# Kernel tuning notes

Measured on AMD Instinct MI355X. Metric: run time of the kernel, lower is better.

The kernel has to match this reference:

```python
import jax, jax.numpy as jnp
import numpy as np

N = 4096; B = 32; LATENT = 16; UNITS = 64; NNZ = 65536; K = 2; M = 2 * K + 1

def _spmm(rows, cols, vals, x):
    # sparse [N,N] @ dense [N,FB] via gather + segment_sum
    return jax.ops.segment_sum(vals[:, None] * x[cols], rows, num_segments=N)

def _gconv(y, supports, W, b):
    # y: (B, N*F) -> Chebyshev-style diffusion over each support, then dense projection
    F = y.shape[1] // N
    x0 = y.reshape(B, N, F).transpose(1, 2, 0).reshape(N, F * B)
    xs = [x0]
    for rows, cols, vals in supports:
        x1 = _spmm(rows, cols, vals, x0)
        xs.append(x1)
        xk1, xk2 = x1, x0
        for _ in range(2, K + 1):
            x2 = 2.0 * _spmm(rows, cols, vals, xk1) - xk2
            xs.append(x2)
            xk1, xk2 = x2, xk1
    # [M,N,F,B] -> [B,N,F,M] -> [B*N, F*M], matching torch permute/reshape
    x = jnp.stack(xs).reshape(M, N, F, B).transpose(3, 1, 2, 0).reshape(B * N, F * M)
    return (x @ W + b).reshape(B, N * W.shape[1])

def setup_inputs():
    key = jax.random.key(0)
    ks = jax.random.split(key, 8)
    r = jax.random.randint(ks[0], (NNZ,), 0, N)
    c = jax.random.randint(ks[1], (NNZ,), 0, N)
    v = jax.random.uniform(ks[2], (NNZ,)) + 0.1
    d_row = jax.ops.segment_sum(v, r, num_segments=N)
    d_col = jax.ops.segment_sum(v, c, num_segments=N)
    inv_row = jnp.where(d_row > 0, 1.0 / d_row, 0.0)
    inv_col = jnp.where(d_col > 0, 1.0 / d_col, 0.0)
    # support1 = (D_out^{-1} A)^T ; support2 = (D_in^{-1} A^T)^T  (COO triples)
    s1_rows, s1_cols, s1_vals = c, r, v * inv_row[r]
    s2_rows, s2_cols, s2_vals = r, c, v * inv_col[c]
    def xavier(k, shape):
        scale = np.sqrt(2.0 / (shape[0] + shape[1])).astype(np.float32)
        return jax.random.normal(k, shape, dtype=jnp.float32) * scale
    return {
        "t_local": 0,
        "y": jax.random.normal(ks[3], (B, N * LATENT), dtype=jnp.float32),
        "W_theta": xavier(ks[4], (LATENT * M, LATENT)),
        "b_lat": jnp.ones((LATENT,), jnp.float32),  # bias_start=1.0; shared (LayerParams keys biases by length)
        "W_hid": xavier(ks[5], (LATENT * M, UNITS)),
        "b_hid": jnp.zeros((UNITS,), jnp.float32),
        "W_out": xavier(ks[6], (UNITS * M, LATENT)),
        "s1_rows": s1_rows, "s1_cols": s1_cols, "s1_vals": s1_vals,
        "s2_rows": s2_rows, "s2_cols": s2_cols, "s2_vals": s2_vals,
    }

def reference(t_local, y, W_theta, b_lat, W_hid, b_hid, W_out,
              s1_rows, s1_cols, s1_vals, s2_rows, s2_cols, s2_vals):
    supports = [(s1_rows, s1_cols, s1_vals), (s2_rows, s2_cols, s2_vals)]
    theta = jax.nn.sigmoid(_gconv(y, supports, W_theta, b_lat))
    c = jnp.tanh(_gconv(y, supports, W_hid, b_hid))   # gen_layers = 1
    c = jnp.tanh(_gconv(c, supports, W_out, b_lat))   # shared bias of length latent_dim
    return -theta * c
```

## Files before the change

### kernel.cpp

```cpp
#include <hip/hip_runtime.h>
#include <stdint.h>

#define NN    4096
#define BB    32
#define NNZE  65536
#define WA    512
#define WB    2048
#define WD    512

typedef __attribute__((ext_vector_type(8))) short bf16x8;
typedef __attribute__((ext_vector_type(4))) float f32x4;

__device__ __forceinline__ float bf2f(unsigned int h) {
    union { unsigned int u; float f; } c; c.u = h << 16; return c.f;
}
__device__ __forceinline__ unsigned int f2bf(float f) {
    union { float ff; unsigned int u; } c; c.ff = f;
    return (c.u + 0x7fffu + ((c.u >> 16) & 1u)) >> 16;
}

__global__ void hist2_kernel(const int* __restrict__ r1, const int* __restrict__ r2,
                             int* __restrict__ cnt1, int* __restrict__ cnt2) {
    int e = blockIdx.x * blockDim.x + threadIdx.x;
    if (e < NNZE) atomicAdd(&cnt1[r1[e]], 1);
    else          atomicAdd(&cnt2[r2[e - NNZE]], 1);
}

__global__ void scan2_kernel(int* cur1, int* rp1, int* cur2, int* rp2) {
    int* cur = (blockIdx.x == 0) ? cur1 : cur2;
    int* rp  = (blockIdx.x == 0) ? rp1  : rp2;
    __shared__ int part[256];
    int t = threadIdx.x;
    int base = t * 16;
    int loc[16];
    int s = 0;
#pragma unroll
    for (int i = 0; i < 16; ++i) { loc[i] = s; s += cur[base + i]; }
    part[t] = s;
    __syncthreads();
    for (int off = 1; off < 256; off <<= 1) {
        int v = 0;
        if (t >= off) v = part[t - off];
        __syncthreads();
        part[t] += v;
        __syncthreads();
    }
    int excl = (t == 0) ? 0 : part[t - 1];
#pragma unroll
    for (int i = 0; i < 16; ++i) rp[base + i] = excl + loc[i];
    __syncthreads();
#pragma unroll
    for (int i = 0; i < 16; ++i) cur[base + i] = rp[base + i];
    if (t == 255) rp[4096] = part[255];
}

__global__ void scatter2_kernel(const int* __restrict__ r1, const int* __restrict__ c1, const float* __restrict__ v1,
                                const int* __restrict__ r2, const int* __restrict__ c2, const float* __restrict__ v2,
                                int* __restrict__ cur1, int* __restrict__ cur2,
                                int* __restrict__ ecol1, float* __restrict__ eval1,
                                int* __restrict__ ecol2, float* __restrict__ eval2) {
    int e = blockIdx.x * blockDim.x + threadIdx.x;
    if (e < NNZE) {
        int pos = atomicAdd(&cur1[r1[e]], 1);
        ecol1[pos] = c1[e]; eval1[pos] = v1[e];
    } else {
        int ee = e - NNZE;
        int pos = atomicAdd(&cur2[r2[ee]], 1);
        ecol2[pos] = c2[ee]; eval2[pos] = v2[ee];
    }
}

__global__ void transA_kernel(const float* __restrict__ y, unsigned short* __restrict__ x0h) {
    int t = threadIdx.x, n = blockIdx.x;
    int b = t & 31, q = t >> 5;
    float4 y4 = *(const float4*)(y + (size_t)b * (NN * 16) + n * 16 + 4 * q);
    uint2 o;
    o.x = f2bf(y4.x) | (f2bf(y4.y) << 16);
    o.y = f2bf(y4.z) | (f2bf(y4.w) << 16);
    *(uint2*)(x0h + (size_t)n * WA + b * 16 + 4 * q) = o;
}

struct SpmmDesc {
    const unsigned short* in;
    const unsigned short* prev;
    float* outF;
    unsigned short* outH;
    const int* rp; const int* ecol; const float* eval;
    float alpha, beta;
};

__launch_bounds__(64)
__global__ void spmmD_kernel(SpmmDesc q0, SpmmDesc q1, SpmmDesc q2, SpmmDesc q3, int ninst) {
    __shared__ int scol[64];
    __shared__ float sval[64];
    int blk = blockIdx.x;
    int xcd = blk & 7;
    int idx = blk >> 3;
    int spx = 8 / ninst;
    int inst = xcd / spx;
    int sub  = xcd - inst * spx;
    int row  = sub * (NN / spx) + idx;
    SpmmDesc q = (inst == 0) ? q0 : (inst == 1) ? q1 : (inst == 2) ? q2 : q3;
    int t = threadIdx.x;
    int beg = q.rp[row], end = q.rp[row + 1];
    float acc[8];
#pragma unroll
    for (int k = 0; k < 8; ++k) acc[k] = 0.f;
    for (int i0 = beg; i0 < end; i0 += 64) {
        int nn = end - i0; if (nn > 64) nn = 64;
        __syncthreads();
        if (t < nn) { scol[t] = q.ecol[i0 + t]; sval[t] = q.eval[i0 + t]; }
        __syncthreads();
#pragma unroll 4
        for (int j = 0; j < nn; ++j) {
            uint4 xv = ((const uint4*)(q.in + (size_t)scol[j] * WD))[t];
            float v = sval[j];
            acc[0] += v * bf2f(xv.x & 0xffffu);
            acc[1] += v * bf2f(xv.x >> 16);
            acc[2] += v * bf2f(xv.y & 0xffffu);
            acc[3] += v * bf2f(xv.y >> 16);
            acc[4] += v * bf2f(xv.z & 0xffffu);
            acc[5] += v * bf2f(xv.z >> 16);
            acc[6] += v * bf2f(xv.w & 0xffffu);
            acc[7] += v * bf2f(xv.w >> 16);
        }
    }
    float r[8];
#pragma unroll
    for (int k = 0; k < 8; ++k) r[k] = q.alpha * acc[k];
    if (q.prev) {
        uint4 pv = ((const uint4*)(q.prev + (size_t)row * WD))[t];
        r[0] += q.beta * bf2f(pv.x & 0xffffu);
        r[1] += q.beta * bf2f(pv.x >> 16);
        r[2] += q.beta * bf2f(pv.y & 0xffffu);
        r[3] += q.beta * bf2f(pv.y >> 16);
        r[4] += q.beta * bf2f(pv.z & 0xffffu);
        r[5] += q.beta * bf2f(pv.z >> 16);
        r[6] += q.beta * bf2f(pv.w & 0xffffu);
        r[7] += q.beta * bf2f(pv.w >> 16);
    }
    if (q.outF) {
        float* po = q.outF + (size_t)row * WD + t * 8;
        *(float4*)(po)     = make_float4(r[0], r[1], r[2], r[3]);
        *(float4*)(po + 4) = make_float4(r[4], r[5], r[6], r[7]);
    } else {
        uint4 o;
        o.x = f2bf(r[0]) | (f2bf(r[1]) << 16);
        o.y = f2bf(r[2]) | (f2bf(r[3]) << 16);
        o.z = f2bf(r[4]) | (f2bf(r[5]) << 16);
        o.w = f2bf(r[6]) | (f2bf(r[7]) << 16);
        ((uint4*)(q.outH + (size_t)row * WD))[t] = o;
    }
}

__launch_bounds__(256)
__global__ void projA_mfma(const unsigned short* __restrict__ xh,
                           const float* __restrict__ Wtheta, const float* __restrict__ Whid,
                           const float* __restrict__ b_hid,
                           float* __restrict__ theta,
                           unsigned short* __restrict__ c) {
    __shared__ __align__(16) unsigned short sW[80 * 104];
    int t = threadIdx.x;
    for (int i = t; i < 80 * 96; i += 256) {
        int col = i / 96, k = i - col * 96;
        int m = k >> 4, f = k & 15;
        float v = 0.f;
        if (m < 5) v = (col < 16) ? Wtheta[(f * 5 + m) * 16 + col]
                                  : Whid[(f * 5 + m) * 64 + (col - 16)];
        sW[col * 104 + k] = (unsigned short)f2bf(v);
    }
    __syncthreads();
    int lane = t & 63, w = t >> 6;
    int r = lane & 15, g = lane >> 4;
    bf16x8 wf[5][3];
#pragma unroll
    for (int ct = 0; ct < 5; ++ct)
#pragma unroll
        for (int kt = 0; kt < 3; ++kt)
            wf[ct][kt] = *(const bf16x8*)(sW + (ct * 16 + r) * 104 + kt * 32 + g * 8);
    float bh[4];
#pragma unroll
    for (int ct = 0; ct < 4; ++ct) bh[ct] = b_hid[ct * 16 + r];

    for (int i = 0; i < 2; ++i) {
        int n = blockIdx.x * 8 + w * 2 + i;
        f32x4 acc[2][5];
#pragma unroll
        for (int bt = 0; bt < 2; ++bt)
#pragma unroll
            for (int ct = 0; ct < 5; ++ct)
                acc[bt][ct] = (f32x4){0.f, 0.f, 0.f, 0.f};
#pragma unroll
        for (int kt = 0; kt < 3; ++kt) {
            bf16x8 a[2];
            int m = kt * 2 + (g >> 1);
#pragma unroll
            for (int bt = 0; bt < 2; ++bt) {
                bf16x8 av = {0, 0, 0, 0, 0, 0, 0, 0};
                if (m < 5)
                    av = *(const bf16x8*)(xh + ((size_t)m * NN + n) * WA
                                          + (bt * 16 + r) * 16 + (g & 1) * 8);
                a[bt] = av;
            }
#pragma unroll
            for (int bt = 0; bt < 2; ++bt)
#pragma unroll
                for (int ct = 0; ct < 5; ++ct)
                    acc[bt][ct] = __builtin_amdgcn_mfma_f32_16x16x32_bf16(
                        a[bt], wf[ct][kt], acc[bt][ct], 0, 0, 0);
        }
#pragma unroll
        for (int bt = 0; bt < 2; ++bt) {
#pragma unroll
            for (int reg = 0; reg < 4; ++reg) {
                int b = bt * 16 + g * 4 + reg;
                theta[(size_t)n * 512 + b * 16 + r] = acc[bt][0][reg];
            }
#pragma unroll
            for (int ct = 1; ct < 5; ++ct) {
                int u = (ct - 1) * 16 + r;
#pragma unroll
                for (int reg = 0; reg < 4; ++reg) {
                    int b = bt * 16 + g * 4 + reg;
                    float hv = tanhf(acc[bt][ct][reg] + bh[ct - 1]);
                    c[(size_t)n * WB + b * 64 + u] = (unsigned short)f2bf(hv);
                }
            }
        }
    }
}

__launch_bounds__(256)
__global__ void preproj_mfma(const unsigned short* __restrict__ c,
                             const float* __restrict__ Wout,
                             float* __restrict__ d0,
                             unsigned short* __restrict__ dd1, unsigned short* __restrict__ dd2,
                             unsigned short* __restrict__ dd3, unsigned short* __restrict__ dd4) {
    __shared__ __align__(16) unsigned short sW[80 * 72];
    int t = threadIdx.x;
    for (int i = t; i < 80 * 64; i += 256) {
        int col = i >> 6, k = i & 63;
        int m = col >> 4, up = col & 15;
        sW[col * 72 + k] = (unsigned short)f2bf(Wout[(k * 5 + m) * 16 + up]);
    }
    __syncthreads();
    int lane = t & 63, w = t >> 6;
    int r = lane & 15, g = lane >> 4;
    bf16x8 wf[5][2];
#pragma unroll
    for (int ct = 0; ct < 5; ++ct)
#pragma unroll
        for (int kt = 0; kt < 2; ++kt)
            wf[ct][kt] = *(const bf16x8*)(sW + (ct * 16 + r) * 72 + kt * 32 + g * 8);

    for (int i = 0; i < 2; ++i) {
        int n = blockIdx.x * 8 + w * 2 + i;
        f32x4 acc[2][5];
#pragma unroll
        for (int bt = 0; bt < 2; ++bt)
#pragma unroll
            for (int ct = 0; ct < 5; ++ct)
                acc[bt][ct] = (f32x4){0.f, 0.f, 0.f, 0.f};
#pragma unroll
        for (int kt = 0; kt < 2; ++kt) {
            bf16x8 a[2];
#pragma unroll
            for (int bt = 0; bt < 2; ++bt)
                a[bt] = *(const bf16x8*)(c + (size_t)n * WB + (bt * 16 + r) * 64
                                         + kt * 32 + g * 8);
#pragma unroll
            for (int bt = 0; bt < 2; ++bt)
#pragma unroll
                for (int ct = 0; ct < 5; ++ct)
                    acc[bt][ct] = __builtin_amdgcn_mfma_f32_16x16x32_bf16(
                        a[bt], wf[ct][kt], acc[bt][ct], 0, 0, 0);
        }
#pragma unroll
        for (int bt = 0; bt < 2; ++bt) {
#pragma unroll
            for (int reg = 0; reg < 4; ++reg) {
                int b = bt * 16 + g * 4 + reg;
                d0[(size_t)n * WD + b * 16 + r] = acc[bt][0][reg];
            }
#pragma unroll
            for (int ct = 1; ct < 5; ++ct) {
                unsigned short* dp = (ct == 1) ? dd1 : (ct == 2) ? dd2 : (ct == 3) ? dd3 : dd4;
#pragma unroll
                for (int reg = 0; reg < 4; ++reg) {
                    int b = bt * 16 + g * 4 + reg;
                    dp[(size_t)n * WD + b * 16 + r] = (unsigned short)f2bf(acc[bt][ct][reg]);
                }
            }
        }
    }
}

__global__ void final2_kernel(const float* __restrict__ theta, const float* __restrict__ d0,
                              const float* __restrict__ w1, const float* __restrict__ z2,
                              const float* __restrict__ w3, const float* __restrict__ z4,
                              const float* __restrict__ b_lat, float* __restrict__ out) {
    int i4 = blockIdx.x * blockDim.x + threadIdx.x;
    size_t i = (size_t)i4 * 4;
    int u = (int)(i & 15);
    int b = (int)((i >> 4) & 31);
    int n = (int)(i >> 9);
    float4 tv = *(const float4*)(theta + i);
    float4 a0 = *(const float4*)(d0 + i);
    float4 a1 = *(const float4*)(w1 + i);
    float4 a2 = *(const float4*)(z2 + i);
    float4 a3 = *(const float4*)(w3 + i);
    float4 a4 = *(const float4*)(z4 + i);
    float4 bl = *(const float4*)(b_lat + u);
    float sx = a0.x + a1.x + a2.x + a3.x + a4.x + bl.x;
    float sy = a0.y + a1.y + a2.y + a3.y + a4.y + bl.y;
    float sz = a0.z + a1.z + a2.z + a3.z + a4.z + bl.z;
    float sw = a0.w + a1.w + a2.w + a3.w + a4.w + bl.w;
    float4 res;
    res.x = -(1.f / (1.f + expf(-(tv.x + bl.x)))) * tanhf(sx);
    res.y = -(1.f / (1.f + expf(-(tv.y + bl.y)))) * tanhf(sy);
    res.z = -(1.f / (1.f + expf(-(tv.z + bl.z)))) * tanhf(sz);
    res.w = -(1.f / (1.f + expf(-(tv.w + bl.w)))) * tanhf(sw);
    *(float4*)(out + ((size_t)b * NN + n) * 16 + u) = res;
}

extern "C" void kernel_launch(void* const* d_in, const int* in_sizes, int n_in,
                              void* d_out, int out_size, void* d_ws, size_t ws_size,
                              hipStream_t stream) {
    const float* y      = (const float*)d_in[1];
    const float* Wtheta = (const float*)d_in[2];
    const float* b_lat  = (const float*)d_in[3];
    const float* Whid   = (const float*)d_in[4];
    const float* b_hid  = (const float*)d_in[5];
    const float* Wout   = (const float*)d_in[6];
    const int*   r1     = (const int*)d_in[7];
    const int*   c1     = (const int*)d_in[8];
    const float* v1     = (const float*)d_in[9];
    const int*   r2     = (const int*)d_in[10];
    const int*   c2     = (const int*)d_in[11];
    const float* v2     = (const float*)d_in[12];
    float* out = (float*)d_out;

    char* ws = (char*)d_ws;
    size_t off = 0;
    auto alloc = [&](size_t bytes) -> char* {
        char* p = ws + off;
        off += (bytes + 255) & ~(size_t)255;
        return p;
    };
    int*   rp1   = (int*)alloc(4097 * 4);
    int*   rp2   = (int*)alloc(4097 * 4);
    int*   cur1  = (int*)alloc(4096 * 4);
    int*   cur2  = (int*)alloc(4096 * 4);
    int*   ecol1 = (int*)alloc(NNZE * 4);
    float* eval1 = (float*)alloc(NNZE * 4);
    int*   ecol2 = (int*)alloc(NNZE * 4);
    float* eval2 = (float*)alloc(NNZE * 4);
    unsigned short* xh = (unsigned short*)alloc((size_t)5 * NN * WA * 2);
    float* theta = (float*)alloc((size_t)NN * 512 * 4);
    char*  creg  = alloc((size_t)NN * WB * 2);
    float* d0 = (float*)alloc((size_t)NN * WD * 4);
    unsigned short* w2h = (unsigned short*)alloc((size_t)NN * WD * 2);
    unsigned short* w4h = (unsigned short*)alloc((size_t)NN * WD * 2);
    float* z2 = (float*)alloc((size_t)NN * WD * 4);
    float* z4 = (float*)alloc((size_t)NN * WD * 4);
    if (off > ws_size) return;

    unsigned short* x0h = xh;
    unsigned short* x1h = xh + (size_t)1 * NN * WA;
    unsigned short* x2h = xh + (size_t)2 * NN * WA;
    unsigned short* x3h = xh + (size_t)3 * NN * WA;
    unsigned short* x4h = xh + (size_t)4 * NN * WA;
    unsigned short* cbuf = (unsigned short*)creg;
    unsigned short* dd1 = (unsigned short*)((char*)xh + ((size_t)0  << 20));
    unsigned short* dd2 = (unsigned short*)((char*)xh + ((size_t)4  << 20));
    unsigned short* dd3 = (unsigned short*)((char*)xh + ((size_t)8  << 20));
    unsigned short* dd4 = (unsigned short*)((char*)xh + ((size_t)12 << 20));
    float* w1 = (float*)creg;
    float* w3 = (float*)(creg + ((size_t)8 << 20));

    hipMemsetAsync(cur1, 0, 2 * 4096 * 4, stream);
    hist2_kernel<<<2 * NNZE / 256, 256, 0, stream>>>(r1, r2, cur1, cur2);
    scan2_kernel<<<2, 256, 0, stream>>>(cur1, rp1, cur2, rp2);
    scatter2_kernel<<<2 * NNZE / 256, 256, 0, stream>>>(r1, c1, v1, r2, c2, v2,
                                                        cur1, cur2, ecol1, eval1, ecol2, eval2);

    transA_kernel<<<NN, 128, 0, stream>>>(y, x0h);
    {
        SpmmDesc a0 = { x0h, nullptr, nullptr, x1h, rp1, ecol1, eval1, 1.f, 0.f };
        SpmmDesc a1 = { x0h, nullptr, nullptr, x3h, rp2, ecol2, eval2, 1.f, 0.f };
        spmmD_kernel<<<2 * NN, 64, 0, stream>>>(a0, a1, a0, a1, 2);
    }
    {
        SpmmDesc a0 = { x1h, x0h, nullptr, x2h, rp1, ecol1, eval1, 2.f, -1.f };
        SpmmDesc a1 = { x3h, x0h, nullptr, x4h, rp2, ecol2, eval2, 2.f, -1.f };
        spmmD_kernel<<<2 * NN, 64, 0, stream>>>(a0, a1, a0, a1, 2);
    }
    projA_mfma<<<NN / 8, 256, 0, stream>>>(xh, Wtheta, Whid, b_hid, theta, cbuf);

    preproj_mfma<<<NN / 8, 256, 0, stream>>>(cbuf, Wout, d0, dd1, dd2, dd3, dd4);
    {
        SpmmDesc a0 = { dd1, nullptr, w1, nullptr, rp1, ecol1, eval1, 1.f, 0.f };
        SpmmDesc a1 = { dd2, nullptr, nullptr, w2h, rp1, ecol1, eval1, 1.f, 0.f };
        SpmmDesc a2 = { dd3, nullptr, w3, nullptr, rp2, ecol2, eval2, 1.f, 0.f };
        SpmmDesc a3 = { dd4, nullptr, nullptr, w4h, rp2, ecol2, eval2, 1.f, 0.f };
        spmmD_kernel<<<4 * NN, 64, 0, stream>>>(a0, a1, a2, a3, 4);
    }
    {
        SpmmDesc b0 = { w2h, dd2, z2, nullptr, rp1, ecol1, eval1, 2.f, -1.f };
        SpmmDesc b1 = { w4h, dd4, z4, nullptr, rp2, ecol2, eval2, 2.f, -1.f };
        spmmD_kernel<<<2 * NN, 64, 0, stream>>>(b0, b1, b0, b1, 2);
    }

    final2_kernel<<<(NN * WD) / 4 / 256, 256, 0, stream>>>(theta, d0, w1, z2, w3, z4, b_lat, out);
}
```

Baseline: 219.4 us.

## Refactor final diffusion via Horner-style SpMM chain and fuse into epilogue

Rewrites the last graph-conv's Chebyshev sum so each support needs one SpMM producing g = 2·S·dd2 + dd1 and a second SpMM applied to g, removing one SpMM pass per support plus the fp32 intermediates w1/w3/z2/z4. The second SpMM over both supports is fused with the sigmoid/tanh epilogue, which also removes the separate final elementwise kernel and its six full-size reads. In exchange, the intermediate g is kept in bf16, which can add rounding error. Each row's combined work now runs in one 64-thread block across both supports, giving fewer and longer blocks.

```diff
diff --git a/kernel.cpp b/kernel.cpp
--- a/kernel.cpp
+++ b/kernel.cpp
@@ -295,32 +295,75 @@
     }
 }
 
-__global__ void final2_kernel(const float* __restrict__ theta, const float* __restrict__ d0,
-                              const float* __restrict__ w1, const float* __restrict__ z2,
-                              const float* __restrict__ w3, const float* __restrict__ z4,
-                              const float* __restrict__ b_lat, float* __restrict__ out) {
-    int i4 = blockIdx.x * blockDim.x + threadIdx.x;
-    size_t i = (size_t)i4 * 4;
-    int u = (int)(i & 15);
-    int b = (int)((i >> 4) & 31);
-    int n = (int)(i >> 9);
-    float4 tv = *(const float4*)(theta + i);
-    float4 a0 = *(const float4*)(d0 + i);
-    float4 a1 = *(const float4*)(w1 + i);
-    float4 a2 = *(const float4*)(z2 + i);
-    float4 a3 = *(const float4*)(w3 + i);
-    float4 a4 = *(const float4*)(z4 + i);
-    float4 bl = *(const float4*)(b_lat + u);
-    float sx = a0.x + a1.x + a2.x + a3.x + a4.x + bl.x;
-    float sy = a0.y + a1.y + a2.y + a3.y + a4.y + bl.y;
-    float sz = a0.z + a1.z + a2.z + a3.z + a4.z + bl.z;
-    float sw = a0.w + a1.w + a2.w + a3.w + a4.w + bl.w;
-    float4 res;
-    res.x = -(1.f / (1.f + expf(-(tv.x + bl.x)))) * tanhf(sx);
-    res.y = -(1.f / (1.f + expf(-(tv.y + bl.y)))) * tanhf(sy);
-    res.z = -(1.f / (1.f + expf(-(tv.z + bl.z)))) * tanhf(sz);
-    res.w = -(1.f / (1.f + expf(-(tv.w + bl.w)))) * tanhf(sw);
-    *(float4*)(out + ((size_t)b * NN + n) * 16 + u) = res;
+__launch_bounds__(64)
+__global__ void finalspmm_kernel(const unsigned short* __restrict__ g1, const unsigned short* __restrict__ g3,
+                                 const int* __restrict__ rp1, const int* __restrict__ ecol1, const float* __restrict__ eval1,
+                                 const int* __restrict__ rp2, const int* __restrict__ ecol2, const float* __restrict__ eval2,
+                                 const float* __restrict__ theta, const float* __restrict__ d0,
+                                 const unsigned short* __restrict__ dd2, const unsigned short* __restrict__ dd4,
+                                 const float* __restrict__ b_lat, float* __restrict__ out) {
+    __shared__ int scol[64];
+    __shared__ float sval[64];
+    int blk = blockIdx.x;
+    int row = (blk & 7) * 512 + (blk >> 3);
+    int t = threadIdx.x;
+    float h[8];
+#pragma unroll
+    for (int k = 0; k < 8; ++k) h[k] = 0.f;
+#pragma unroll
+    for (int s = 0; s < 2; ++s) {
+        const int* rp = s ? rp2 : rp1;
+        const int* ecol = s ? ecol2 : ecol1;
+        const float* eval = s ? eval2 : eval1;
+        const unsigned short* gin = s ? g3 : g1;
+        int beg = rp[row], end = rp[row + 1];
+        for (int i0 = beg; i0 < end; i0 += 64) {
+            int nn = end - i0; if (nn > 64) nn = 64;
+            __syncthreads();
+            if (t < nn) { scol[t] = ecol[i0 + t]; sval[t] = eval[i0 + t]; }
+            __syncthreads();
+#pragma unroll 4
+            for (int j = 0; j < nn; ++j) {
+                uint4 xv = ((const uint4*)(gin + (size_t)scol[j] * WD))[t];
+                float v = sval[j];
+                h[0] += v * bf2f(xv.x & 0xffffu);
+                h[1] += v * bf2f(xv.x >> 16);
+                h[2] += v * bf2f(xv.y & 0xffffu);
+                h[3] += v * bf2f(xv.y >> 16);
+                h[4] += v * bf2f(xv.z & 0xffffu);
+                h[5] += v * bf2f(xv.z >> 16);
+                h[6] += v * bf2f(xv.w & 0xffffu);
+                h[7] += v * bf2f(xv.w >> 16);
+            }
+        }
+    }
+    size_t base = (size_t)row * WD + t * 8;
+    float4 dA = *(const float4*)(d0 + base);
+    float4 dB = *(const float4*)(d0 + base + 4);
+    uint4 p2 = *(const uint4*)(dd2 + base);
+    uint4 p4 = *(const uint4*)(dd4 + base);
+    float4 tA = *(const float4*)(theta + base);
+    float4 tB = *(const float4*)(theta + base + 4);
+    float4 blA = *(const float4*)(b_lat + (t & 1) * 8);
+    float4 blB = *(const float4*)(b_lat + (t & 1) * 8 + 4);
+    float tot[8], th[8];
+    tot[0] = dA.x - bf2f(p2.x & 0xffffu) - bf2f(p4.x & 0xffffu) + h[0] + blA.x;
+    tot[1] = dA.y - bf2f(p2.x >> 16)     - bf2f(p4.x >> 16)     + h[1] + blA.y;
+    tot[2] = dA.z - bf2f(p2.y & 0xffffu) - bf2f(p4.y & 0xffffu) + h[2] + blA.z;
+    tot[3] = dA.w - bf2f(p2.y >> 16)     - bf2f(p4.y >> 16)     + h[3] + blA.w;
+    tot[4] = dB.x - bf2f(p2.z & 0xffffu) - bf2f(p4.z & 0xffffu) + h[4] + blB.x;
+    tot[5] = dB.y - bf2f(p2.z >> 16)     - bf2f(p4.z >> 16)     + h[5] + blB.y;
+    tot[6] = dB.z - bf2f(p2.w & 0xffffu) - bf2f(p4.w & 0xffffu) + h[6] + blB.z;
+    tot[7] = dB.w - bf2f(p2.w >> 16)     - bf2f(p4.w >> 16)     + h[7] + blB.w;
+    th[0] = tA.x + blA.x; th[1] = tA.y + blA.y; th[2] = tA.z + blA.z; th[3] = tA.w + blA.w;
+    th[4] = tB.x + blB.x; th[5] = tB.y + blB.y; th[6] = tB.z + blB.z; th[7] = tB.w + blB.w;
+    float res[8];
+#pragma unroll
+    for (int j = 0; j < 8; ++j)
+        res[j] = -(1.f / (1.f + expf(-th[j]))) * tanhf(tot[j]);
+    float* po = out + ((size_t)(t >> 1) * NN + row) * 16 + (t & 1) * 8;
+    *(float4*)(po)     = make_float4(res[0], res[1], res[2], res[3]);
+    *(float4*)(po + 4) = make_float4(res[4], res[5], res[6], res[7]);
 }
 
 extern "C" void kernel_launch(void* const* d_in, const int* in_sizes, int n_in,
@@ -359,10 +402,8 @@
     float* theta = (float*)alloc((size_t)NN * 512 * 4);
     char*  creg  = alloc((size_t)NN * WB * 2);
     float* d0 = (float*)alloc((size_t)NN * WD * 4);
-    unsigned short* w2h = (unsigned short*)alloc((size_t)NN * WD * 2);
-    unsigned short* w4h = (unsigned short*)alloc((size_t)NN * WD * 2);
-    float* z2 = (float*)alloc((size_t)NN * WD * 4);
-    float* z4 = (float*)alloc((size_t)NN * WD * 4);
+    unsigned short* g1 = (unsigned short*)alloc((size_t)NN * WD * 2);
+    unsigned short* g3 = (unsigned short*)alloc((size_t)NN * WD * 2);
     if (off > ws_size) return;
 
     unsigned short* x0h = xh;
@@ -375,8 +416,6 @@
     unsigned short* dd2 = (unsigned short*)((char*)xh + ((size_t)4  << 20));
     unsigned short* dd3 = (unsigned short*)((char*)xh + ((size_t)8  << 20));
     unsigned short* dd4 = (unsigned short*)((char*)xh + ((size_t)12 << 20));
-    float* w1 = (float*)creg;
-    float* w3 = (float*)(creg + ((size_t)8 << 20));
 
     hipMemsetAsync(cur1, 0, 2 * 4096 * 4, stream);
     hist2_kernel<<<2 * NNZE / 256, 256, 0, stream>>>(r1, r2, cur1, cur2);
@@ -399,17 +438,10 @@
 
     preproj_mfma<<<NN / 8, 256, 0, stream>>>(cbuf, Wout, d0, dd1, dd2, dd3, dd4);
     {
-        SpmmDesc a0 = { dd1, nullptr, w1, nullptr, rp1, ecol1, eval1, 1.f, 0.f };
-        SpmmDesc a1 = { dd2, nullptr, nullptr, w2h, rp1, ecol1, eval1, 1.f, 0.f };
-        SpmmDesc a2 = { dd3, nullptr, w3, nullptr, rp2, ecol2, eval2, 1.f, 0.f };
-        SpmmDesc a3 = { dd4, nullptr, nullptr, w4h, rp2, ecol2, eval2, 1.f, 0.f };
-        spmmD_kernel<<<4 * NN, 64, 0, stream>>>(a0, a1, a2, a3, 4);
-    }
-    {
-        SpmmDesc b0 = { w2h, dd2, z2, nullptr, rp1, ecol1, eval1, 2.f, -1.f };
-        SpmmDesc b1 = { w4h, dd4, z4, nullptr, rp2, ecol2, eval2, 2.f, -1.f };
-        spmmD_kernel<<<2 * NN, 64, 0, stream>>>(b0, b1, b0, b1, 2);
-    }
-
-    final2_kernel<<<(NN * WD) / 4 / 256, 256, 0, stream>>>(theta, d0, w1, z2, w3, z4, b_lat, out);
-}
+        SpmmDesc a0 = { dd2, dd1, nullptr, g1, rp1, ecol1, eval1, 2.f, 1.f };
+        SpmmDesc a1 = { dd4, dd3, nullptr, g3, rp2, ecol2, eval2, 2.f, 1.f };
+        spmmD_kernel<<<2 * NN, 64, 0, stream>>>(a0, a1, a0, a1, 2);
+    }
+    finalspmm_kernel<<<NN, 64, 0, stream>>>(g1, g3, rp1, ecol1, eval1, rp2, ecol2, eval2,
+                                            theta, d0, dd2, dd4, b_lat, out);
+}
```

After: 208.3 us. 5.1% less time.
